# Performance work log

Measured on AMD Instinct MI355X. Metric: run time of the kernel, lower is better.

The kernel has to match this reference:

```python
import jax, jax.numpy as jnp
import numpy as np

N = 50000
E_RAND = 800000
IN, HID, OUT = 128, 64, 40
HEADS = (2, 1, 1)
NEG_SLOPE = 0.2


def setup_inputs() -> dict:
    key = jax.random.key(0)
    ks = jax.random.split(key, 16)
    # random edges with src != dst, then append self-loops (remove+add_self_loop)
    src_r = jax.random.randint(ks[0], (E_RAND,), 0, N)
    off = jax.random.randint(ks[1], (E_RAND,), 1, N)
    dst_r = (src_r + off) % N
    loops = jnp.arange(N)
    src = jnp.concatenate([src_r, loops]).astype(jnp.int64)
    dst = jnp.concatenate([dst_r, loops]).astype(jnp.int64)
    in_feat = jax.random.normal(ks[2], (N, IN), dtype=jnp.float32)

    def lin(k, fan_in, fan_out):
        return jax.random.normal(k, (fan_in, fan_out), dtype=jnp.float32) / np.sqrt(fan_in)

    H0, H1, H2 = HEADS
    # layer 0: in=IN, out=HID, heads=H0
    W0 = lin(ks[3], IN, H0 * HID)
    al0 = jax.random.normal(ks[4], (H0, HID), dtype=jnp.float32) * 0.1
    ar0 = jax.random.normal(ks[5], (H0, HID), dtype=jnp.float32) * 0.1
    b0 = jnp.zeros((H0 * HID,), dtype=jnp.float32)
    # layer 1: in=HID*H0, out=HID, heads=H1
    W1 = lin(ks[6], HID * H0, H1 * HID)
    al1 = jax.random.normal(ks[7], (H1, HID), dtype=jnp.float32) * 0.1
    ar1 = jax.random.normal(ks[8], (H1, HID), dtype=jnp.float32) * 0.1
    b1 = jnp.zeros((H1 * HID,), dtype=jnp.float32)
    # layer 2: in=HID*H1, out=OUT, heads=H2
    W2 = lin(ks[9], HID * H1, H2 * OUT)
    al2 = jax.random.normal(ks[10], (H2, OUT), dtype=jnp.float32) * 0.1
    ar2 = jax.random.normal(ks[11], (H2, OUT), dtype=jnp.float32) * 0.1
    b2 = jnp.zeros((H2 * OUT,), dtype=jnp.float32)
    return {"in_feat": in_feat, "src": src, "dst": dst,
            "W0": W0, "al0": al0, "ar0": ar0, "b0": b0,
            "W1": W1, "al1": al1, "ar1": ar1, "b1": b1,
            "W2": W2, "al2": al2, "ar2": ar2, "b2": b2}


def _gat_layer(x, src, dst, W, al, ar, b):
    # x: [N, Fin]; W: [Fin, H*D]; al/ar: [H, D]; b: [H*D]
    H, D = al.shape
    feat = (x @ W).reshape(-1, H, D)                 # [N, H, D]
    el = jnp.sum(feat * al, axis=-1)                 # [N, H]
    er = jnp.sum(feat * ar, axis=-1)                 # [N, H]
    e = jax.nn.leaky_relu(el[src] + er[dst], NEG_SLOPE)  # [E, H]
    m = jax.ops.segment_max(e, dst, num_segments=x.shape[0])
    ee = jnp.exp(e - jax.lax.stop_gradient(m)[dst])
    s = jax.ops.segment_sum(ee, dst, num_segments=x.shape[0])
    alpha = ee / s[dst]                              # softmax over in-edges per dst
    out = jax.ops.segment_sum(feat[src] * alpha[:, :, None], dst,
                              num_segments=x.shape[0])  # [N, H, D]
    return out + b.reshape(1, H, D)


def reference(in_feat, src, dst, W0, al0, ar0, b0, W1, al1, ar1, b1, W2, al2, ar2, b2):
    h = _gat_layer(in_feat, src, dst, W0, al0, ar0, b0).reshape(in_feat.shape[0], -1)  # flatten(1)
    h = _gat_layer(h, src, dst, W1, al1, ar1, b1).mean(axis=1)                          # mean over heads
    h = _gat_layer(h, src, dst, W2, al2, ar2, b2).reshape(in_feat.shape[0], -1)         # flatten(1)
    return h
```

## Files before the change

kernel.cpp:

```cpp
#include <hip/hip_runtime.h>
#include <hip/hip_fp16.h>
#include <math.h>

#define NEG_SLOPE 0.2f

typedef _Float16 h8 __attribute__((ext_vector_type(8)));
typedef float f4 __attribute__((ext_vector_type(4)));


__device__ inline float2 up2(unsigned u) {
    __half2 h;
    __builtin_memcpy(&h, &u, 4);
    return __half22float2(h);
}
__device__ inline unsigned pk2(float a, float b) {
    __half2 h = __floats2half2_rn(a, b);
    unsigned u;
    __builtin_memcpy(&u, &h, 4);
    return u;
}
__device__ inline void fma8(float* acc, const uint4& v, float p) {
    float2 f;
    f = up2(v.x); acc[0] += f.x * p; acc[1] += f.y * p;
    f = up2(v.y); acc[2] += f.x * p; acc[3] += f.y * p;
    f = up2(v.z); acc[4] += f.x * p; acc[5] += f.y * p;
    f = up2(v.w); acc[6] += f.x * p; acc[7] += f.y * p;
}
__device__ inline float dot4(const float4& a, const float4& b) {
    return a.x * b.x + a.y * b.y + a.z * b.z + a.w * b.w;
}


__global__ __launch_bounds__(256) void prep(const float* __restrict__ W0,
                                            const float* __restrict__ W1,
                                            const float* __restrict__ W2,
                                            const float* __restrict__ al2,
                                            const float* __restrict__ ar2,
                                            __half* __restrict__ P0,
                                            __half* __restrict__ P1,
                                            __half* __restrict__ P2,
                                            float* __restrict__ al2p,
                                            float* __restrict__ ar2p,
                                            int* __restrict__ deg, int N) {
    int b = blockIdx.x;
    int gtid = b * 256 + threadIdx.x;
    for (int i = gtid; i < N; i += gridDim.x * 256) deg[i] = 0;

    if (b < 14) {
        const float* W;
        __half* P;
        int K, M, Msrc, lb = b;
        if (lb < 8) {
            W = W0; P = P0; K = 128; M = 128; Msrc = 128;
        } else if (lb < 12) {
            W = W1; P = P1; K = 128; M = 64; Msrc = 64; lb -= 8;
        } else {
            W = W2; P = P2; K = 64; M = 64; Msrc = 40; lb -= 12;
        }
        int t = lb * 256 + threadIdx.x;
        int nk8 = K >> 3;
        if (t < M * nk8) {
            int m = t % M, k8 = t / M;
            int k = k8 * 8;
            int c = m >> 4, s = k >> 5, hi = (k >> 3) & 3, lane = hi * 16 + (m & 15);
            float v[8];
#pragma unroll
            for (int i = 0; i < 8; ++i)
                v[i] = (m < Msrc) ? W[(size_t)(k + i) * Msrc + m] : 0.f;
            uint4 o;
            o.x = pk2(v[0], v[1]);
            o.y = pk2(v[2], v[3]);
            o.z = pk2(v[4], v[5]);
            o.w = pk2(v[6], v[7]);
            *(uint4*)(P + (size_t)((c * (K >> 5) + s) * 64 + lane) * 8) = o;
        }
    } else if (b == 14) {
        int t = threadIdx.x;
        if (t < 64) {
            al2p[t] = (t < 40) ? al2[t] : 0.f;
            ar2p[t] = (t < 40) ? ar2[t] : 0.f;
        }
    }
}


__global__ __launch_bounds__(256) void degree_hist_rank(const int* __restrict__ dst,
                                                        int* __restrict__ deg,
                                                        int* __restrict__ rank, int E) {
    int e = blockIdx.x * blockDim.x + threadIdx.x;
    if (e >= E) return;
    int d = __builtin_nontemporal_load(&dst[e]);
    int r = atomicAdd(&deg[d], 1);
    __builtin_nontemporal_store(r, &rank[e]);
}

__global__ __launch_bounds__(256) void scan_block_sums(const int* __restrict__ in,
                                                       int* __restrict__ partial, int n) {
    int i = blockIdx.x * 256 + threadIdx.x;
    int v = (i < n) ? in[i] : 0;
#pragma unroll
    for (int off = 32; off; off >>= 1) v += __shfl_xor(v, off);
    __shared__ int wsum[4];
    if ((threadIdx.x & 63) == 0) wsum[threadIdx.x >> 6] = v;
    __syncthreads();
    if (threadIdx.x == 0) partial[blockIdx.x] = wsum[0] + wsum[1] + wsum[2] + wsum[3];
}

__global__ __launch_bounds__(256) void scan_final2(const int* __restrict__ in,
                                                   const int* __restrict__ partial,
                                                   int* __restrict__ out, int n) {
    __shared__ int buf[256];
    __shared__ int wsum[4];
    int t = threadIdx.x;
    int i = blockIdx.x * 256 + t;
    int v = (i < n) ? in[i] : 0;
    buf[t] = v;
    __syncthreads();
    for (int off = 1; off < 256; off <<= 1) {
        int x = (t >= off) ? buf[t - off] : 0;
        __syncthreads();
        buf[t] += x;
        __syncthreads();
    }
    int incl = buf[t];
    int pv = (t < blockIdx.x) ? partial[t] : 0;
#pragma unroll
    for (int off = 32; off; off >>= 1) pv += __shfl_xor(pv, off);
    if ((t & 63) == 0) wsum[t >> 6] = pv;
    __syncthreads();
    int pre = wsum[0] + wsum[1] + wsum[2] + wsum[3];
    if (i < n) out[i] = pre + incl - v;
    if (i == n - 1) out[n] = pre + incl;
}

__global__ __launch_bounds__(256) void scatter_rank(const int* __restrict__ src,
                                                    const int* __restrict__ dst,
                                                    const int* __restrict__ rank,
                                                    const int* __restrict__ row_start,
                                                    int* __restrict__ csr_src, int E) {
    int e = blockIdx.x * blockDim.x + threadIdx.x;
    if (e >= E) return;
    int d = __builtin_nontemporal_load(&dst[e]);
    int s = __builtin_nontemporal_load(&src[e]);
    int r = __builtin_nontemporal_load(&rank[e]);
    csr_src[row_start[d] + r] = s;
}


template <int K, int M, int H, bool A16>
__global__ __launch_bounds__(256) void gemm_mfma(const void* __restrict__ xin,
                                                 const __half* __restrict__ Wp,
                                                 const float* __restrict__ al,
                                                 const float* __restrict__ ar,
                                                 __half* __restrict__ outh,
                                                 float* __restrict__ el,
                                                 float* __restrict__ er, int N) {
    constexpr int KS = K / 32;
    constexpr int CF = M / 16;
    constexpr int LDT = 133;
    constexpr int CH8 = M / 8;
    constexpr int NC8 = CH8 / 4;
    __shared__ float tl[4 * 16 * LDT];
    const int tid = threadIdx.x;
    const int wid = tid >> 6, lane = tid & 63;
    const int lhi = lane >> 4, llo = lane & 15;
    const int rowbase = blockIdx.x * 64 + wid * 16;
    float* wt = tl + wid * 16 * LDT;

    f4 acc[CF];
#pragma unroll
    for (int c = 0; c < CF; ++c) acc[c] = f4{0.f, 0.f, 0.f, 0.f};

    const int arow = rowbase + llo;
    const bool aval = arow < N;
#pragma unroll
    for (int s = 0; s < KS; ++s) {
        h8 a = {};
        if (aval) {
            if constexpr (A16) {
                const __half* xp = (const __half*)xin + (size_t)arow * K + s * 32 + lhi * 8;
                a = *(const h8*)xp;
            } else {
                const float4* xp = (const float4*)((const float*)xin + (size_t)arow * K +
                                                   s * 32 + lhi * 8);
                float4 x0 = xp[0];
                float4 x1 = xp[1];
                a[0] = (_Float16)x0.x; a[1] = (_Float16)x0.y;
                a[2] = (_Float16)x0.z; a[3] = (_Float16)x0.w;
                a[4] = (_Float16)x1.x; a[5] = (_Float16)x1.y;
                a[6] = (_Float16)x1.z; a[7] = (_Float16)x1.w;
            }
        }
#pragma unroll
        for (int c = 0; c < CF; ++c) {
            h8 b = *(const h8*)(Wp + (size_t)((c * KS + s) * 64 + lane) * 8);
            acc[c] = __builtin_amdgcn_mfma_f32_16x16x32_f16(a, b, acc[c], 0, 0, 0);
        }
    }

#pragma unroll
    for (int c = 0; c < CF; ++c) {
#pragma unroll
        for (int r = 0; r < 4; ++r)
            wt[(lhi * 4 + r) * LDT + c * 16 + llo] = acc[c][r];
    }

    const int rrow = lane >> 2;
    const int q = lane & 3;
    const int grow = rowbase + rrow;
    float elp[H], erp[H];
#pragma unroll
    for (int h = 0; h < H; ++h) { elp[h] = 0.f; erp[h] = 0.f; }
    const float4* al4 = (const float4*)al;
    const float4* ar4 = (const float4*)ar;
#pragma unroll
    for (int i = 0; i < NC8; ++i) {
        int j8 = q + 4 * i;
        float4 v0 = *(float4*)&wt[rrow * LDT + 8 * j8];
        float4 v1 = *(float4*)&wt[rrow * LDT + 8 * j8 + 4];
        int h = (H == 2 && i >= NC8 / 2) ? 1 : 0;
        float4 a0 = al4[2 * j8], a1 = al4[2 * j8 + 1];
        float4 r0 = ar4[2 * j8], r1 = ar4[2 * j8 + 1];
        elp[h] += dot4(v0, a0) + dot4(v1, a1);
        erp[h] += dot4(v0, r0) + dot4(v1, r1);
        if (grow < N) {
            uint4 pkv;
            pkv.x = pk2(v0.x, v0.y);
            pkv.y = pk2(v0.z, v0.w);
            pkv.z = pk2(v1.x, v1.y);
            pkv.w = pk2(v1.z, v1.w);
            *(uint4*)(outh + (size_t)grow * M + 8 * j8) = pkv;
        }
    }
#pragma unroll
    for (int h = 0; h < H; ++h) {
#pragma unroll
        for (int off = 1; off < 4; off <<= 1) {
            elp[h] += __shfl_xor(elp[h], off);
            erp[h] += __shfl_xor(erp[h], off);
        }
    }
    if (q == 0 && grow < N) {
        if constexpr (H == 2) {
            *(float2*)&el[(size_t)grow * 2] = float2{elp[0], elp[1]};
            *(float2*)&er[(size_t)grow * 2] = float2{erp[0], erp[1]};
        } else {
            el[grow] = elp[0];
            er[grow] = erp[0];
        }
    }
}


template <int H, int D, int FSTRIDE, int T, bool OUT16>
__global__ __launch_bounds__(256) void gat_aggregate2(const __half* __restrict__ feat,
                                                      const float* __restrict__ el,
                                                      const float* __restrict__ er,
                                                      const int* __restrict__ row_start,
                                                      const int* __restrict__ csr_src,
                                                      const float* __restrict__ bias,
                                                      void* __restrict__ out, int N) {
    constexpr int NLp = FSTRIDE / 8;
    constexpr int GnH = 32 / NLp;
    constexpr int BATCH = GnH * T;
    constexpr int WL = (H * D) / 8;
    static_assert(32 % NLp == 0 && BATCH <= 32, "layout");
    int pair = (blockIdx.x * blockDim.x + threadIdx.x) >> 6;
    int lane = threadIdx.x & 63;
    if (pair * 2 >= N) return;
    const int l32 = lane & 31;
    const int hb = lane & 32;
    const int dstn = pair * 2 + (lane >> 5);
    const bool dval = dstn < N;
    int beg = dval ? row_start[dstn] : 0;
    int end = dval ? row_start[dstn + 1] : 0;
    int cnt = end - beg;

    float er_d[H];
#pragma unroll
    for (int h = 0; h < H; ++h) er_d[h] = dval ? er[(size_t)dstn * H + h] : 0.f;

    float ssum[H];
    float acc8[8];
#pragma unroll
    for (int h = 0; h < H; ++h) ssum[h] = 0.f;
#pragma unroll
    for (int i = 0; i < 8; ++i) acc8[i] = 0.f;

    const int g = l32 / NLp;
    const int ln = l32 % NLp;

    int trips = (cnt + 31) >> 5;
    {
        int to = __shfl_xor(trips, 32);
        trips = (to > trips) ? to : trips;
    }

    for (int it = 0; it < trips; ++it) {
        int base = beg + it * 32;
        int idx = base + l32;
        bool valid = idx < end;
        int s = csr_src[valid ? idx : beg];
        float p[H];
        if constexpr (H == 2) {
            float2 e2 = ((const float2*)el)[s];
            float e0 = e2.x + er_d[0];
            float e1 = e2.y + er_d[1];
            e0 = (e0 > 0.f) ? e0 : NEG_SLOPE * e0;
            e1 = (e1 > 0.f) ? e1 : NEG_SLOPE * e1;
            p[0] = valid ? __expf(e0) : 0.f;
            p[1] = valid ? __expf(e1) : 0.f;
            ssum[0] += p[0];
            ssum[1] += p[1];
        } else {
            float e = el[s] + er_d[0];
            e = (e > 0.f) ? e : NEG_SLOPE * e;
            p[0] = valid ? __expf(e) : 0.f;
            ssum[0] += p[0];
        }
        int cc = end - base;
        cc = (cc < 0) ? 0 : ((cc > 32) ? 32 : cc);
        int ccm = cc;
        {
            int o = __shfl_xor(ccm, 32);
            ccm = (o > ccm) ? o : ccm;
        }
        for (int j = 0; j < ccm; j += BATCH) {
            uint4 v[T];
#pragma unroll
            for (int t = 0; t < T; ++t) {
                if (j + GnH * t < cc) {
                    int sj = __shfl(s, hb + j + GnH * t + g);
                    v[t] = ((const uint4*)(feat + (size_t)sj * FSTRIDE))[ln];
                }
            }
#pragma unroll
            for (int t = 0; t < T; ++t) {
                if (j + GnH * t < cc) {
                    int slot = hb + j + GnH * t + g;
                    float pj = __shfl(p[0], slot);
                    if constexpr (H == 2) {
                        float pj1 = __shfl(p[1], slot);
                        pj = (ln >= 8) ? pj1 : pj;
                    }
                    fma8(acc8, v[t], pj);
                }
            }
        }
    }

#pragma unroll
    for (int h = 0; h < H; ++h)
#pragma unroll
        for (int off = 16; off; off >>= 1) ssum[h] += __shfl_xor(ssum[h], off);
#pragma unroll
    for (int i = 0; i < 8; ++i) {
#pragma unroll
        for (int off = NLp; off < 32; off <<= 1) acc8[i] += __shfl_xor(acc8[i], off);
    }
    if (l32 < WL && dval) {
        float inv;
        if constexpr (H == 2) inv = 1.f / ((l32 >= 8) ? ssum[1] : ssum[0]);
        else inv = 1.f / ssum[0];
        const float4* bp = (const float4*)bias;
        float4 bv0 = bp[2 * l32], bv1 = bp[2 * l32 + 1];
        float4 o0, o1;
        o0.x = acc8[0] * inv + bv0.x; o0.y = acc8[1] * inv + bv0.y;
        o0.z = acc8[2] * inv + bv0.z; o0.w = acc8[3] * inv + bv0.w;
        o1.x = acc8[4] * inv + bv1.x; o1.y = acc8[5] * inv + bv1.y;
        o1.z = acc8[6] * inv + bv1.z; o1.w = acc8[7] * inv + bv1.w;
        if constexpr (OUT16) {
            __half* op = (__half*)out + (size_t)dstn * (H * D);
            uint4 pkv;
            pkv.x = pk2(o0.x, o0.y);
            pkv.y = pk2(o0.z, o0.w);
            pkv.z = pk2(o1.x, o1.y);
            pkv.w = pk2(o1.z, o1.w);
            ((uint4*)op)[l32] = pkv;
        } else {
            float4* op = (float4*)((float*)out + (size_t)dstn * (H * D));
            op[2 * l32] = o0;
            op[2 * l32 + 1] = o1;
        }
    }
}


extern "C" void kernel_launch(void* const* d_in, const int* in_sizes, int n_in,
                              void* d_out, int out_size, void* d_ws, size_t ws_size,
                              hipStream_t stream) {
    const float* in_feat = (const float*)d_in[0];
    const int*   src     = (const int*)d_in[1];
    const int*   dst     = (const int*)d_in[2];
    const float* W0 = (const float*)d_in[3];
    const float* al0 = (const float*)d_in[4];
    const float* ar0 = (const float*)d_in[5];
    const float* b0 = (const float*)d_in[6];
    const float* W1 = (const float*)d_in[7];
    const float* al1 = (const float*)d_in[8];
    const float* ar1 = (const float*)d_in[9];
    const float* b1 = (const float*)d_in[10];
    const float* W2 = (const float*)d_in[11];
    const float* al2 = (const float*)d_in[12];
    const float* ar2 = (const float*)d_in[13];
    const float* b2 = (const float*)d_in[14];
    float* out = (float*)d_out;

    const int N = in_sizes[0] / 128;
    const int E = in_sizes[1];

    char* ws = (char*)d_ws;
    auto alloc = [&](size_t bytes) -> void* {
        void* p = (void*)ws;
        ws += (bytes + 255) & ~(size_t)255;
        return p;
    };
    int* deg       = (int*)alloc((size_t)N * 4);
    int* row_start = (int*)alloc((size_t)(N + 1) * 4);
    int* csr_src   = (int*)alloc((size_t)E * 4);
    int* rank      = (int*)alloc((size_t)E * 4);
    int* partial   = (int*)alloc(256 * 4);
    __half* feat   = (__half*)alloc((size_t)N * 128 * 2);
    float* el      = (float*)alloc((size_t)N * 2 * 4);
    float* er      = (float*)alloc((size_t)N * 2 * 4);
    __half* h0h    = (__half*)alloc((size_t)N * 128 * 2);
    __half* h1h    = (__half*)alloc((size_t)N * 64 * 2);
    __half* Wp0    = (__half*)alloc((size_t)128 * 128 * 2);
    __half* Wp1    = (__half*)alloc((size_t)128 * 64 * 2);
    __half* Wp2    = (__half*)alloc((size_t)64 * 64 * 2);
    float* al2p    = (float*)alloc(64 * 4);
    float* ar2p    = (float*)alloc(64 * 4);

    int egrid = (E + 255) / 256;
    int nb = (N + 255) / 256;

    prep<<<256, 256, 0, stream>>>(W0, W1, W2, al2, ar2, Wp0, Wp1, Wp2, al2p, ar2p, deg, N);
    degree_hist_rank<<<egrid, 256, 0, stream>>>(dst, deg, rank, E);
    scan_block_sums<<<nb, 256, 0, stream>>>(deg, partial, N);
    scan_final2<<<nb, 256, 0, stream>>>(deg, partial, row_start, N);
    scatter_rank<<<egrid, 256, 0, stream>>>(src, dst, rank, row_start, csr_src, E);

    int npairs = (N + 1) / 2;
    int pgrid = (npairs * 64 + 255) / 256;
    int mgrid = (N + 63) / 64;

    gemm_mfma<128, 128, 2, false><<<mgrid, 256, 0, stream>>>(in_feat, Wp0, al0, ar0, feat, el, er, N);
    gat_aggregate2<2, 64, 128, 8, true><<<pgrid, 256, 0, stream>>>(feat, el, er, row_start, csr_src, b0, h0h, N);

    gemm_mfma<128, 64, 1, true><<<mgrid, 256, 0, stream>>>(h0h, Wp1, al1, ar1, feat, el, er, N);
    gat_aggregate2<1, 64, 64, 8, true><<<pgrid, 256, 0, stream>>>(feat, el, er, row_start, csr_src, b1, h1h, N);

    gemm_mfma<64, 64, 1, true><<<mgrid, 256, 0, stream>>>(h1h, Wp2, al2p, ar2p, feat, el, er, N);
    gat_aggregate2<1, 40, 64, 8, false><<<pgrid, 256, 0, stream>>>(feat, el, er, row_start, csr_src, b2, out, N);
}
```

Measured before the change: 281.5 us.

## Fuse whole GAT pipeline into one cooperative persistent kernel with grid syncs

Replaces the chain of roughly ten separate launches (weight prep, degree histogram, scan, CSR scatter, three GEMMs and three aggregations) with a single cooperative kernel. The stages are separated by grid.sync() and use grid-stride loops, with a grid sized from occupancy and capped at 1024 blocks. The layer-0 GEMM is also placed in the same phase as the degree histogram so the two overlap. This removes per-launch overhead and the gaps between kernels, but the grid is capped and each barrier is a device-wide sync. The multi-kernel path is kept as a fallback if the cooperative launch fails.

Result: slower. 373.5 us (+32.7%).

```diff
diff --git a/kernel.cpp b/kernel.cpp
--- a/kernel.cpp
+++ b/kernel.cpp
@@ -1,6 +1,9 @@
 #include <hip/hip_runtime.h>
+#include <hip/hip_cooperative_groups.h>
 #include <hip/hip_fp16.h>
 #include <math.h>
+
+namespace cg = cooperative_groups;
 
 #define NEG_SLOPE 0.2f
 
@@ -28,6 +31,371 @@
 }
 __device__ inline float dot4(const float4& a, const float4& b) {
     return a.x * b.x + a.y * b.y + a.z * b.z + a.w * b.w;
+}
+
+
+template <int K, int M, int H, bool A16>
+__device__ void dev_gemm(float* tl_base, const void* __restrict__ xin,
+                         const __half* __restrict__ Wp,
+                         const float* __restrict__ al,
+                         const float* __restrict__ ar,
+                         __half* __restrict__ outh,
+                         float* __restrict__ el,
+                         float* __restrict__ er, int N) {
+    constexpr int KS = K / 32;
+    constexpr int CF = M / 16;
+    constexpr int LDT = 133;
+    constexpr int CH8 = M / 8;
+    constexpr int NC8 = CH8 / 4;
+    const int tid = threadIdx.x;
+    const int wid = tid >> 6, lane = tid & 63;
+    const int lhi = lane >> 4, llo = lane & 15;
+    float* wt = tl_base + wid * 16 * LDT;
+    const float4* al4 = (const float4*)al;
+    const float4* ar4 = (const float4*)ar;
+    const int ntiles = (N + 63) >> 6;
+
+    for (int tile = blockIdx.x; tile < ntiles; tile += gridDim.x) {
+        const int rowbase = tile * 64 + wid * 16;
+        f4 acc[CF];
+#pragma unroll
+        for (int c = 0; c < CF; ++c) acc[c] = f4{0.f, 0.f, 0.f, 0.f};
+
+        const int arow = rowbase + llo;
+        const bool aval = arow < N;
+#pragma unroll
+        for (int s = 0; s < KS; ++s) {
+            h8 a = {};
+            if (aval) {
+                if constexpr (A16) {
+                    const __half* xp = (const __half*)xin + (size_t)arow * K + s * 32 + lhi * 8;
+                    a = *(const h8*)xp;
+                } else {
+                    const float4* xp = (const float4*)((const float*)xin + (size_t)arow * K +
+                                                       s * 32 + lhi * 8);
+                    float4 x0 = xp[0];
+                    float4 x1 = xp[1];
+                    a[0] = (_Float16)x0.x; a[1] = (_Float16)x0.y;
+                    a[2] = (_Float16)x0.z; a[3] = (_Float16)x0.w;
+                    a[4] = (_Float16)x1.x; a[5] = (_Float16)x1.y;
+                    a[6] = (_Float16)x1.z; a[7] = (_Float16)x1.w;
+                }
+            }
+#pragma unroll
+            for (int c = 0; c < CF; ++c) {
+                h8 b = *(const h8*)(Wp + (size_t)((c * KS + s) * 64 + lane) * 8);
+                acc[c] = __builtin_amdgcn_mfma_f32_16x16x32_f16(a, b, acc[c], 0, 0, 0);
+            }
+        }
+
+#pragma unroll
+        for (int c = 0; c < CF; ++c) {
+#pragma unroll
+            for (int r = 0; r < 4; ++r)
+                wt[(lhi * 4 + r) * LDT + c * 16 + llo] = acc[c][r];
+        }
+
+        const int rrow = lane >> 2;
+        const int q = lane & 3;
+        const int grow = rowbase + rrow;
+        float elp[H], erp[H];
+#pragma unroll
+        for (int h = 0; h < H; ++h) { elp[h] = 0.f; erp[h] = 0.f; }
+#pragma unroll
+        for (int i = 0; i < NC8; ++i) {
+            int j8 = q + 4 * i;
+            float4 v0 = *(float4*)&wt[rrow * LDT + 8 * j8];
+            float4 v1 = *(float4*)&wt[rrow * LDT + 8 * j8 + 4];
+            int h = (H == 2 && i >= NC8 / 2) ? 1 : 0;
+            float4 a0 = al4[2 * j8], a1 = al4[2 * j8 + 1];
+            float4 r0 = ar4[2 * j8], r1 = ar4[2 * j8 + 1];
+            elp[h] += dot4(v0, a0) + dot4(v1, a1);
+            erp[h] += dot4(v0, r0) + dot4(v1, r1);
+            if (grow < N) {
+                uint4 pkv;
+                pkv.x = pk2(v0.x, v0.y);
+                pkv.y = pk2(v0.z, v0.w);
+                pkv.z = pk2(v1.x, v1.y);
+                pkv.w = pk2(v1.z, v1.w);
+                *(uint4*)(outh + (size_t)grow * M + 8 * j8) = pkv;
+            }
+        }
+#pragma unroll
+        for (int h = 0; h < H; ++h) {
+#pragma unroll
+            for (int off = 1; off < 4; off <<= 1) {
+                elp[h] += __shfl_xor(elp[h], off);
+                erp[h] += __shfl_xor(erp[h], off);
+            }
+        }
+        if (q == 0 && grow < N) {
+            if constexpr (H == 2) {
+                *(float2*)&el[(size_t)grow * 2] = float2{elp[0], elp[1]};
+                *(float2*)&er[(size_t)grow * 2] = float2{erp[0], erp[1]};
+            } else {
+                el[grow] = elp[0];
+                er[grow] = erp[0];
+            }
+        }
+    }
+}
+
+
+template <int H, int D, int FSTRIDE, int T, bool OUT16>
+__device__ void dev_agg(const __half* __restrict__ feat,
+                        const float* __restrict__ el,
+                        const float* __restrict__ er,
+                        const int* __restrict__ row_start,
+                        const int* __restrict__ csr_src,
+                        const float* __restrict__ bias,
+                        void* __restrict__ out, int N) {
+    constexpr int NLp = FSTRIDE / 8;
+    constexpr int GnH = 32 / NLp;
+    constexpr int BATCH = GnH * T;
+    constexpr int WL = (H * D) / 8;
+    static_assert(32 % NLp == 0 && BATCH <= 32, "layout");
+    const int lane = threadIdx.x & 63;
+    const int wid = threadIdx.x >> 6;
+    const int l32 = lane & 31;
+    const int hb = lane & 32;
+    const int g = l32 / NLp;
+    const int ln = l32 % NLp;
+    const int npairs = (N + 1) >> 1;
+
+    for (int pair = blockIdx.x * 4 + wid; pair < npairs; pair += gridDim.x * 4) {
+        const int dstn = pair * 2 + (lane >> 5);
+        const bool dval = dstn < N;
+        int beg = dval ? row_start[dstn] : 0;
+        int end = dval ? row_start[dstn + 1] : 0;
+        int cnt = end - beg;
+
+        float er_d[H];
+#pragma unroll
+        for (int h = 0; h < H; ++h) er_d[h] = dval ? er[(size_t)dstn * H + h] : 0.f;
+
+        float ssum[H];
+        float acc8[8];
+#pragma unroll
+        for (int h = 0; h < H; ++h) ssum[h] = 0.f;
+#pragma unroll
+        for (int i = 0; i < 8; ++i) acc8[i] = 0.f;
+
+        int trips = (cnt + 31) >> 5;
+        {
+            int to = __shfl_xor(trips, 32);
+            trips = (to > trips) ? to : trips;
+        }
+
+        for (int it = 0; it < trips; ++it) {
+            int base = beg + it * 32;
+            int idx = base + l32;
+            bool valid = idx < end;
+            int s = csr_src[valid ? idx : beg];
+            float p[H];
+            if constexpr (H == 2) {
+                float2 e2 = ((const float2*)el)[s];
+                float e0 = e2.x + er_d[0];
+                float e1 = e2.y + er_d[1];
+                e0 = (e0 > 0.f) ? e0 : NEG_SLOPE * e0;
+                e1 = (e1 > 0.f) ? e1 : NEG_SLOPE * e1;
+                p[0] = valid ? __expf(e0) : 0.f;
+                p[1] = valid ? __expf(e1) : 0.f;
+                ssum[0] += p[0];
+                ssum[1] += p[1];
+            } else {
+                float e = el[s] + er_d[0];
+                e = (e > 0.f) ? e : NEG_SLOPE * e;
+                p[0] = valid ? __expf(e) : 0.f;
+                ssum[0] += p[0];
+            }
+            int cc = end - base;
+            cc = (cc < 0) ? 0 : ((cc > 32) ? 32 : cc);
+            int ccm = cc;
+            {
+                int o = __shfl_xor(ccm, 32);
+                ccm = (o > ccm) ? o : ccm;
+            }
+            for (int j = 0; j < ccm; j += BATCH) {
+                uint4 v[T];
+#pragma unroll
+                for (int t = 0; t < T; ++t) {
+                    if (j + GnH * t < cc) {
+                        int sj = __shfl(s, hb + j + GnH * t + g);
+                        v[t] = ((const uint4*)(feat + (size_t)sj * FSTRIDE))[ln];
+                    }
+                }
+#pragma unroll
+                for (int t = 0; t < T; ++t) {
+                    if (j + GnH * t < cc) {
+                        int slot = hb + j + GnH * t + g;
+                        float pj = __shfl(p[0], slot);
+                        if constexpr (H == 2) {
+                            float pj1 = __shfl(p[1], slot);
+                            pj = (ln >= 8) ? pj1 : pj;
+                        }
+                        fma8(acc8, v[t], pj);
+                    }
+                }
+            }
+        }
+
+#pragma unroll
+        for (int h = 0; h < H; ++h)
+#pragma unroll
+            for (int off = 16; off; off >>= 1) ssum[h] += __shfl_xor(ssum[h], off);
+#pragma unroll
+        for (int i = 0; i < 8; ++i) {
+#pragma unroll
+            for (int off = NLp; off < 32; off <<= 1) acc8[i] += __shfl_xor(acc8[i], off);
+        }
+        if (l32 < WL && dval) {
+            float inv;
+            if constexpr (H == 2) inv = 1.f / ((l32 >= 8) ? ssum[1] : ssum[0]);
+            else inv = 1.f / ssum[0];
+            const float4* bp = (const float4*)bias;
+            float4 bv0 = bp[2 * l32], bv1 = bp[2 * l32 + 1];
+            float4 o0, o1;
+            o0.x = acc8[0] * inv + bv0.x; o0.y = acc8[1] * inv + bv0.y;
+            o0.z = acc8[2] * inv + bv0.z; o0.w = acc8[3] * inv + bv0.w;
+            o1.x = acc8[4] * inv + bv1.x; o1.y = acc8[5] * inv + bv1.y;
+            o1.z = acc8[6] * inv + bv1.z; o1.w = acc8[7] * inv + bv1.w;
+            if constexpr (OUT16) {
+                __half* op = (__half*)out + (size_t)dstn * (H * D);
+                uint4 pkv;
+                pkv.x = pk2(o0.x, o0.y);
+                pkv.y = pk2(o0.z, o0.w);
+                pkv.z = pk2(o1.x, o1.y);
+                pkv.w = pk2(o1.z, o1.w);
+                ((uint4*)op)[l32] = pkv;
+            } else {
+                float4* op = (float4*)((float*)out + (size_t)dstn * (H * D));
+                op[2 * l32] = o0;
+                op[2 * l32 + 1] = o1;
+            }
+        }
+    }
+}
+
+
+__global__ __launch_bounds__(256) void mega(
+    const float* __restrict__ in_feat, const int* __restrict__ src,
+    const int* __restrict__ dst,
+    const float* __restrict__ W0, const float* __restrict__ al0,
+    const float* __restrict__ ar0, const float* __restrict__ b0,
+    const float* __restrict__ W1, const float* __restrict__ al1,
+    const float* __restrict__ ar1, const float* __restrict__ b1,
+    const float* __restrict__ W2, const float* __restrict__ al2,
+    const float* __restrict__ ar2, const float* __restrict__ b2,
+    float* __restrict__ out,
+    int* __restrict__ deg, int* __restrict__ row_start,
+    int* __restrict__ csr_src, int* __restrict__ rank, int* __restrict__ partial,
+    __half* __restrict__ feat, float* __restrict__ el, float* __restrict__ er,
+    __half* __restrict__ h0h, __half* __restrict__ h1h,
+    __half* __restrict__ Wp0, __half* __restrict__ Wp1, __half* __restrict__ Wp2,
+    float* __restrict__ al2p, float* __restrict__ ar2p, int N, int E) {
+    cg::grid_group grid = cg::this_grid();
+    __shared__ float sm_f[4 * 16 * 133];
+    int* sm_i = (int*)sm_f;
+    const int t = threadIdx.x;
+    const int gt = blockIdx.x * 256 + t;
+    const int gsz = gridDim.x * 256;
+
+    for (int i = gt; i < N; i += gsz) deg[i] = 0;
+    if (blockIdx.x < 14) {
+        const float* W;
+        __half* P;
+        int K, M, Msrc, lb = blockIdx.x;
+        if (lb < 8) {
+            W = W0; P = Wp0; K = 128; M = 128; Msrc = 128;
+        } else if (lb < 12) {
+            W = W1; P = Wp1; K = 128; M = 64; Msrc = 64; lb -= 8;
+        } else {
+            W = W2; P = Wp2; K = 64; M = 64; Msrc = 40; lb -= 12;
+        }
+        int tt = lb * 256 + t;
+        int nk8 = K >> 3;
+        if (tt < M * nk8) {
+            int m = tt % M, k8 = tt / M;
+            int k = k8 * 8;
+            int c = m >> 4, s = k >> 5, hi = (k >> 3) & 3, lane = hi * 16 + (m & 15);
+            float v[8];
+#pragma unroll
+            for (int i = 0; i < 8; ++i)
+                v[i] = (m < Msrc) ? W[(size_t)(k + i) * Msrc + m] : 0.f;
+            uint4 o;
+            o.x = pk2(v[0], v[1]);
+            o.y = pk2(v[2], v[3]);
+            o.z = pk2(v[4], v[5]);
+            o.w = pk2(v[6], v[7]);
+            *(uint4*)(P + (size_t)((c * (K >> 5) + s) * 64 + lane) * 8) = o;
+        }
+    } else if (blockIdx.x == 14 && t < 64) {
+        al2p[t] = (t < 40) ? al2[t] : 0.f;
+        ar2p[t] = (t < 40) ? ar2[t] : 0.f;
+    }
+    grid.sync();
+
+    dev_gemm<128, 128, 2, false>(sm_f, in_feat, Wp0, al0, ar0, feat, el, er, N);
+    for (int e = gt; e < E; e += gsz) {
+        int d = dst[e];
+        rank[e] = atomicAdd(&deg[d], 1);
+    }
+    grid.sync();
+
+    for (int b = blockIdx.x; b * 256 < N; b += gridDim.x) {
+        int i = b * 256 + t;
+        int v = (i < N) ? deg[i] : 0;
+#pragma unroll
+        for (int off = 32; off; off >>= 1) v += __shfl_xor(v, off);
+        if ((t & 63) == 0) sm_i[256 + (t >> 6)] = v;
+        __syncthreads();
+        if (t == 0) partial[b] = sm_i[256] + sm_i[257] + sm_i[258] + sm_i[259];
+        __syncthreads();
+    }
+    grid.sync();
+
+    for (int b = blockIdx.x; b * 256 < N; b += gridDim.x) {
+        int i = b * 256 + t;
+        int v = (i < N) ? deg[i] : 0;
+        sm_i[t] = v;
+        __syncthreads();
+        for (int off = 1; off < 256; off <<= 1) {
+            int x = (t >= off) ? sm_i[t - off] : 0;
+            __syncthreads();
+            sm_i[t] += x;
+            __syncthreads();
+        }
+        int incl = sm_i[t];
+        int pv = (t < b) ? partial[t] : 0;
+#pragma unroll
+        for (int off = 32; off; off >>= 1) pv += __shfl_xor(pv, off);
+        if ((t & 63) == 0) sm_i[256 + (t >> 6)] = pv;
+        __syncthreads();
+        int pre = sm_i[256] + sm_i[257] + sm_i[258] + sm_i[259];
+        if (i < N) row_start[i] = pre + incl - v;
+        if (i == N - 1) row_start[N] = pre + incl;
+        __syncthreads();
+    }
+    grid.sync();
+
+    for (int e = gt; e < E; e += gsz) {
+        csr_src[row_start[dst[e]] + rank[e]] = src[e];
+    }
+    grid.sync();
+
+    dev_agg<2, 64, 128, 8, true>(feat, el, er, row_start, csr_src, b0, h0h, N);
+    grid.sync();
+
+    dev_gemm<128, 64, 1, true>(sm_f, h0h, Wp1, al1, ar1, feat, el, er, N);
+    grid.sync();
+
+    dev_agg<1, 64, 64, 8, true>(feat, el, er, row_start, csr_src, b1, h1h, N);
+    grid.sync();
+
+    dev_gemm<64, 64, 1, true>(sm_f, h1h, Wp2, al2p, ar2p, feat, el, er, N);
+    grid.sync();
+
+    dev_agg<1, 40, 64, 8, false>(feat, el, er, row_start, csr_src, b2, out, N);
 }
 
 
@@ -82,7 +450,6 @@
         }
     }
 }
-
 
 __global__ __launch_bounds__(256) void degree_hist_rank(const int* __restrict__ dst,
                                                         int* __restrict__ deg,
@@ -146,7 +513,6 @@
     csr_src[row_start[d] + r] = s;
 }
 
-
 template <int K, int M, int H, bool A16>
 __global__ __launch_bounds__(256) void gemm_mfma(const void* __restrict__ xin,
                                                  const __half* __restrict__ Wp,
@@ -155,102 +521,9 @@
                                                  __half* __restrict__ outh,
                                                  float* __restrict__ el,
                                                  float* __restrict__ er, int N) {
-    constexpr int KS = K / 32;
-    constexpr int CF = M / 16;
-    constexpr int LDT = 133;
-    constexpr int CH8 = M / 8;
-    constexpr int NC8 = CH8 / 4;
-    __shared__ float tl[4 * 16 * LDT];
-    const int tid = threadIdx.x;
-    const int wid = tid >> 6, lane = tid & 63;
-    const int lhi = lane >> 4, llo = lane & 15;
-    const int rowbase = blockIdx.x * 64 + wid * 16;
-    float* wt = tl + wid * 16 * LDT;
-
-    f4 acc[CF];
-#pragma unroll
-    for (int c = 0; c < CF; ++c) acc[c] = f4{0.f, 0.f, 0.f, 0.f};
-
-    const int arow = rowbase + llo;
-    const bool aval = arow < N;
-#pragma unroll
-    for (int s = 0; s < KS; ++s) {
-        h8 a = {};
-        if (aval) {
-            if constexpr (A16) {
-                const __half* xp = (const __half*)xin + (size_t)arow * K + s * 32 + lhi * 8;
-                a = *(const h8*)xp;
-            } else {
-                const float4* xp = (const float4*)((const float*)xin + (size_t)arow * K +
-                                                   s * 32 + lhi * 8);
-                float4 x0 = xp[0];
-                float4 x1 = xp[1];
-                a[0] = (_Float16)x0.x; a[1] = (_Float16)x0.y;
-                a[2] = (_Float16)x0.z; a[3] = (_Float16)x0.w;
-                a[4] = (_Float16)x1.x; a[5] = (_Float16)x1.y;
-                a[6] = (_Float16)x1.z; a[7] = (_Float16)x1.w;
-            }
-        }
-#pragma unroll
-        for (int c = 0; c < CF; ++c) {
-            h8 b = *(const h8*)(Wp + (size_t)((c * KS + s) * 64 + lane) * 8);
-            acc[c] = __builtin_amdgcn_mfma_f32_16x16x32_f16(a, b, acc[c], 0, 0, 0);
-        }
-    }
-
-#pragma unroll
-    for (int c = 0; c < CF; ++c) {
-#pragma unroll
-        for (int r = 0; r < 4; ++r)
-            wt[(lhi * 4 + r) * LDT + c * 16 + llo] = acc[c][r];
-    }
-
-    const int rrow = lane >> 2;
-    const int q = lane & 3;
-    const int grow = rowbase + rrow;
-    float elp[H], erp[H];
-#pragma unroll
-    for (int h = 0; h < H; ++h) { elp[h] = 0.f; erp[h] = 0.f; }
-    const float4* al4 = (const float4*)al;
-    const float4* ar4 = (const float4*)ar;
-#pragma unroll
-    for (int i = 0; i < NC8; ++i) {
-        int j8 = q + 4 * i;
-        float4 v0 = *(float4*)&wt[rrow * LDT + 8 * j8];
-        float4 v1 = *(float4*)&wt[rrow * LDT + 8 * j8 + 4];
-        int h = (H == 2 && i >= NC8 / 2) ? 1 : 0;
-        float4 a0 = al4[2 * j8], a1 = al4[2 * j8 + 1];
-        float4 r0 = ar4[2 * j8], r1 = ar4[2 * j8 + 1];
-        elp[h] += dot4(v0, a0) + dot4(v1, a1);
-        erp[h] += dot4(v0, r0) + dot4(v1, r1);
-        if (grow < N) {
-            uint4 pkv;
-            pkv.x = pk2(v0.x, v0.y);
-            pkv.y = pk2(v0.z, v0.w);
-            pkv.z = pk2(v1.x, v1.y);
-            pkv.w = pk2(v1.z, v1.w);
-            *(uint4*)(outh + (size_t)grow * M + 8 * j8) = pkv;
-        }
-    }
-#pragma unroll
-    for (int h = 0; h < H; ++h) {
-#pragma unroll
-        for (int off = 1; off < 4; off <<= 1) {
-            elp[h] += __shfl_xor(elp[h], off);
-            erp[h] += __shfl_xor(erp[h], off);
-        }
-    }
-    if (q == 0 && grow < N) {
-        if constexpr (H == 2) {
-            *(float2*)&el[(size_t)grow * 2] = float2{elp[0], elp[1]};
-            *(float2*)&er[(size_t)grow * 2] = float2{erp[0], erp[1]};
-        } else {
-            el[grow] = elp[0];
-            er[grow] = erp[0];
-        }
-    }
-}
-
+    __shared__ float tl[4 * 16 * 133];
+    dev_gemm<K, M, H, A16>(tl, xin, Wp, al, ar, outh, el, er, N);
+}
 
 template <int H, int D, int FSTRIDE, int T, bool OUT16>
 __global__ __launch_bounds__(256) void gat_aggregate2(const __half* __restrict__ feat,
@@ -260,129 +533,7 @@
                                                       const int* __restrict__ csr_src,
                                                       const float* __restrict__ bias,
                                                       void* __restrict__ out, int N) {
-    constexpr int NLp = FSTRIDE / 8;
-    constexpr int GnH = 32 / NLp;
-    constexpr int BATCH = GnH * T;
-    constexpr int WL = (H * D) / 8;
-    static_assert(32 % NLp == 0 && BATCH <= 32, "layout");
-    int pair = (blockIdx.x * blockDim.x + threadIdx.x) >> 6;
-    int lane = threadIdx.x & 63;
-    if (pair * 2 >= N) return;
-    const int l32 = lane & 31;
-    const int hb = lane & 32;
-    const int dstn = pair * 2 + (lane >> 5);
-    const bool dval = dstn < N;
-    int beg = dval ? row_start[dstn] : 0;
-    int end = dval ? row_start[dstn + 1] : 0;
-    int cnt = end - beg;
-
-    float er_d[H];
-#pragma unroll
-    for (int h = 0; h < H; ++h) er_d[h] = dval ? er[(size_t)dstn * H + h] : 0.f;
-
-    float ssum[H];
-    float acc8[8];
-#pragma unroll
-    for (int h = 0; h < H; ++h) ssum[h] = 0.f;
-#pragma unroll
-    for (int i = 0; i < 8; ++i) acc8[i] = 0.f;
-
-    const int g = l32 / NLp;
-    const int ln = l32 % NLp;
-
-    int trips = (cnt + 31) >> 5;
-    {
-        int to = __shfl_xor(trips, 32);
-        trips = (to > trips) ? to : trips;
-    }
-
-    for (int it = 0; it < trips; ++it) {
-        int base = beg + it * 32;
-        int idx = base + l32;
-        bool valid = idx < end;
-        int s = csr_src[valid ? idx : beg];
-        float p[H];
-        if constexpr (H == 2) {
-            float2 e2 = ((const float2*)el)[s];
-            float e0 = e2.x + er_d[0];
-            float e1 = e2.y + er_d[1];
-            e0 = (e0 > 0.f) ? e0 : NEG_SLOPE * e0;
-            e1 = (e1 > 0.f) ? e1 : NEG_SLOPE * e1;
-            p[0] = valid ? __expf(e0) : 0.f;
-            p[1] = valid ? __expf(e1) : 0.f;
-            ssum[0] += p[0];
-            ssum[1] += p[1];
-        } else {
-            float e = el[s] + er_d[0];
-            e = (e > 0.f) ? e : NEG_SLOPE * e;
-            p[0] = valid ? __expf(e) : 0.f;
-            ssum[0] += p[0];
-        }
-        int cc = end - base;
-        cc = (cc < 0) ? 0 : ((cc > 32) ? 32 : cc);
-        int ccm = cc;
-        {
-            int o = __shfl_xor(ccm, 32);
-            ccm = (o > ccm) ? o : ccm;
-        }
-        for (int j = 0; j < ccm; j += BATCH) {
-            uint4 v[T];
-#pragma unroll
-            for (int t = 0; t < T; ++t) {
-                if (j + GnH * t < cc) {
-                    int sj = __shfl(s, hb + j + GnH * t + g);
-                    v[t] = ((const uint4*)(feat + (size_t)sj * FSTRIDE))[ln];
-                }
-            }
-#pragma unroll
-            for (int t = 0; t < T; ++t) {
-                if (j + GnH * t < cc) {
-                    int slot = hb + j + GnH * t + g;
-                    float pj = __shfl(p[0], slot);
-                    if constexpr (H == 2) {
-                        float pj1 = __shfl(p[1], slot);
-                        pj = (ln >= 8) ? pj1 : pj;
-                    }
-                    fma8(acc8, v[t], pj);
-                }
-            }
-        }
-    }
-
-#pragma unroll
-    for (int h = 0; h < H; ++h)
-#pragma unroll
-        for (int off = 16; off; off >>= 1) ssum[h] += __shfl_xor(ssum[h], off);
-#pragma unroll
-    for (int i = 0; i < 8; ++i) {
-#pragma unroll
-        for (int off = NLp; off < 32; off <<= 1) acc8[i] += __shfl_xor(acc8[i], off);
-    }
-    if (l32 < WL && dval) {
-        float inv;
-        if constexpr (H == 2) inv = 1.f / ((l32 >= 8) ? ssum[1] : ssum[0]);
-        else inv = 1.f / ssum[0];
-        const float4* bp = (const float4*)bias;
-        float4 bv0 = bp[2 * l32], bv1 = bp[2 * l32 + 1];
-        float4 o0, o1;
-        o0.x = acc8[0] * inv + bv0.x; o0.y = acc8[1] * inv + bv0.y;
-        o0.z = acc8[2] * inv + bv0.z; o0.w = acc8[3] * inv + bv0.w;
-        o1.x = acc8[4] * inv + bv1.x; o1.y = acc8[5] * inv + bv1.y;
-        o1.z = acc8[6] * inv + bv1.z; o1.w = acc8[7] * inv + bv1.w;
-        if constexpr (OUT16) {
-            __half* op = (__half*)out + (size_t)dstn * (H * D);
-            uint4 pkv;
-            pkv.x = pk2(o0.x, o0.y);
-            pkv.y = pk2(o0.z, o0.w);
-            pkv.z = pk2(o1.x, o1.y);
-            pkv.w = pk2(o1.z, o1.w);
-            ((uint4*)op)[l32] = pkv;
-        } else {
-            float4* op = (float4*)((float*)out + (size_t)dstn * (H * D));
-            op[2 * l32] = o0;
-            op[2 * l32 + 1] = o1;
-        }
-    }
+    dev_agg<H, D, FSTRIDE, T, OUT16>(feat, el, er, row_start, csr_src, bias, out, N);
 }
 
 
@@ -431,6 +582,43 @@
     float* al2p    = (float*)alloc(64 * 4);
     float* ar2p    = (float*)alloc(64 * 4);
 
+    static int coop_grid = -2;
+    if (coop_grid == -2) {
+        int dev_sup = 0;
+        if (hipDeviceGetAttribute(&dev_sup, hipDeviceAttributeCooperativeLaunch, 0) !=
+                hipSuccess ||
+            !dev_sup) {
+            coop_grid = 0;
+        } else {
+            int per_cu = 0;
+            hipError_t e =
+                hipOccupancyMaxActiveBlocksPerMultiprocessor(&per_cu, mega, 256, 0);
+            if (e != hipSuccess || per_cu <= 0) {
+                coop_grid = 0;
+            } else {
+                coop_grid = per_cu * 256;
+                if (coop_grid > 1024) coop_grid = 1024;
+            }
+        }
+    }
+    if (coop_grid > 0) {
+        void* args[] = {
+            (void*)&in_feat, (void*)&src, (void*)&dst,
+            (void*)&W0, (void*)&al0, (void*)&ar0, (void*)&b0,
+            (void*)&W1, (void*)&al1, (void*)&ar1, (void*)&b1,
+            (void*)&W2, (void*)&al2, (void*)&ar2, (void*)&b2,
+            (void*)&out,
+            (void*)&deg, (void*)&row_start, (void*)&csr_src, (void*)&rank,
+            (void*)&partial,
+            (void*)&feat, (void*)&el, (void*)&er, (void*)&h0h, (void*)&h1h,
+            (void*)&Wp0, (void*)&Wp1, (void*)&Wp2, (void*)&al2p, (void*)&ar2p,
+            (void*)&N, (void*)&E};
+        hipError_t e = hipLaunchCooperativeKernel((const void*)mega, dim3(coop_grid),
+                                                  dim3(256), args, 0, stream);
+        if (e == hipSuccess) return;
+        coop_grid = 0;
+    }
+
     int egrid = (E + 255) / 256;
     int nb = (N + 255) / 256;
 
```

## Fuse aggregation with next-layer GEMM and merge CSR scatter with first GEMM

Applied to the files above, without the earlier changes.

Each aggregation kernel now writes its fp16 output tile into swizzled LDS, and the same block runs the next layer's MFMA GEMM on it. This removes the h0/h1 global round-trips and two kernel launches. The CSR build switches from a rank array to atomic cursors, and that scatter is fused into the layer-0 GEMM kernel. The cost is a nondeterministic neighbour order within each CSR row, lower parallelism in the agg_gemm kernels (one block per 64 nodes, 8 serial iterations per wave), and possible load imbalance.

After: 332.1 us. +18.0%, slower.

```diff
diff --git a/kernel.cpp b/kernel.cpp
--- a/kernel.cpp
+++ b/kernel.cpp
@@ -84,14 +84,11 @@
 }
 
 
-__global__ __launch_bounds__(256) void degree_hist_rank(const int* __restrict__ dst,
-                                                        int* __restrict__ deg,
-                                                        int* __restrict__ rank, int E) {
+__global__ __launch_bounds__(256) void hist(const int* __restrict__ dst,
+                                            int* __restrict__ deg, int E) {
     int e = blockIdx.x * blockDim.x + threadIdx.x;
     if (e >= E) return;
-    int d = __builtin_nontemporal_load(&dst[e]);
-    int r = atomicAdd(&deg[d], 1);
-    __builtin_nontemporal_store(r, &rank[e]);
+    atomicAdd(&deg[__builtin_nontemporal_load(&dst[e])], 1);
 }
 
 __global__ __launch_bounds__(256) void scan_block_sums(const int* __restrict__ in,
@@ -106,9 +103,10 @@
     if (threadIdx.x == 0) partial[blockIdx.x] = wsum[0] + wsum[1] + wsum[2] + wsum[3];
 }
 
-__global__ __launch_bounds__(256) void scan_final2(const int* __restrict__ in,
+__global__ __launch_bounds__(256) void scan_final3(const int* __restrict__ in,
                                                    const int* __restrict__ partial,
-                                                   int* __restrict__ out, int n) {
+                                                   int* __restrict__ out,
+                                                   int* __restrict__ cursor, int n) {
     __shared__ int buf[256];
     __shared__ int wsum[4];
     int t = threadIdx.x;
@@ -129,43 +127,30 @@
     if ((t & 63) == 0) wsum[t >> 6] = pv;
     __syncthreads();
     int pre = wsum[0] + wsum[1] + wsum[2] + wsum[3];
-    if (i < n) out[i] = pre + incl - v;
+    if (i < n) {
+        int rs = pre + incl - v;
+        out[i] = rs;
+        cursor[i] = rs;
+    }
     if (i == n - 1) out[n] = pre + incl;
 }
 
-__global__ __launch_bounds__(256) void scatter_rank(const int* __restrict__ src,
-                                                    const int* __restrict__ dst,
-                                                    const int* __restrict__ rank,
-                                                    const int* __restrict__ row_start,
-                                                    int* __restrict__ csr_src, int E) {
-    int e = blockIdx.x * blockDim.x + threadIdx.x;
-    if (e >= E) return;
-    int d = __builtin_nontemporal_load(&dst[e]);
-    int s = __builtin_nontemporal_load(&src[e]);
-    int r = __builtin_nontemporal_load(&rank[e]);
-    csr_src[row_start[d] + r] = s;
-}
-
-
-template <int K, int M, int H, bool A16>
-__global__ __launch_bounds__(256) void gemm_mfma(const void* __restrict__ xin,
-                                                 const __half* __restrict__ Wp,
-                                                 const float* __restrict__ al,
-                                                 const float* __restrict__ ar,
-                                                 __half* __restrict__ outh,
-                                                 float* __restrict__ el,
-                                                 float* __restrict__ er, int N) {
+
+template <int K, int M, int H, int AMODE, int LSTR>
+__device__ __forceinline__ void gemm_tile(float* wt, const void* __restrict__ xin,
+                                          const __half* aw,
+                                          const __half* __restrict__ Wp,
+                                          const float* __restrict__ al,
+                                          const float* __restrict__ ar,
+                                          __half* __restrict__ outh,
+                                          float* __restrict__ el,
+                                          float* __restrict__ er, int rowbase, int N) {
     constexpr int KS = K / 32;
     constexpr int CF = M / 16;
-    constexpr int LDT = 133;
-    constexpr int CH8 = M / 8;
-    constexpr int NC8 = CH8 / 4;
-    __shared__ float tl[4 * 16 * LDT];
-    const int tid = threadIdx.x;
-    const int wid = tid >> 6, lane = tid & 63;
+    constexpr int LDT = (M == 128) ? 133 : 69;
+    constexpr int NC8 = (M / 8) / 4;
+    const int lane = threadIdx.x & 63;
     const int lhi = lane >> 4, llo = lane & 15;
-    const int rowbase = blockIdx.x * 64 + wid * 16;
-    float* wt = tl + wid * 16 * LDT;
 
     f4 acc[CF];
 #pragma unroll
@@ -176,11 +161,14 @@
 #pragma unroll
     for (int s = 0; s < KS; ++s) {
         h8 a = {};
-        if (aval) {
-            if constexpr (A16) {
-                const __half* xp = (const __half*)xin + (size_t)arow * K + s * 32 + lhi * 8;
-                a = *(const h8*)xp;
-            } else {
+        if constexpr (AMODE == 2) {
+            int c8 = s * 4 + lhi;
+            a = *(const h8*)(aw + llo * LSTR + ((c8 ^ (llo & 7)) << 3));
+        } else if constexpr (AMODE == 1) {
+            if (aval)
+                a = *(const h8*)((const __half*)xin + (size_t)arow * K + s * 32 + lhi * 8);
+        } else {
+            if (aval) {
                 const float4* xp = (const float4*)((const float*)xin + (size_t)arow * K +
                                                    s * 32 + lhi * 8);
                 float4 x0 = xp[0];
@@ -197,6 +185,7 @@
             acc[c] = __builtin_amdgcn_mfma_f32_16x16x32_f16(a, b, acc[c], 0, 0, 0);
         }
     }
+    asm volatile("" ::: "memory");
 
 #pragma unroll
     for (int c = 0; c < CF; ++c) {
@@ -204,6 +193,7 @@
         for (int r = 0; r < 4; ++r)
             wt[(lhi * 4 + r) * LDT + c * 16 + llo] = acc[c][r];
     }
+    asm volatile("" ::: "memory");
 
     const int rrow = lane >> 2;
     const int q = lane & 3;
@@ -252,26 +242,25 @@
 }
 
 
-template <int H, int D, int FSTRIDE, int T, bool OUT16>
-__global__ __launch_bounds__(256) void gat_aggregate2(const __half* __restrict__ feat,
-                                                      const float* __restrict__ el,
-                                                      const float* __restrict__ er,
-                                                      const int* __restrict__ row_start,
-                                                      const int* __restrict__ csr_src,
-                                                      const float* __restrict__ bias,
-                                                      void* __restrict__ out, int N) {
+template <int H, int D, int FSTRIDE, int T>
+__device__ __forceinline__ void agg_one(const __half* __restrict__ feat,
+                                        const float* __restrict__ el,
+                                        const float* __restrict__ er,
+                                        const int* __restrict__ row_start,
+                                        const int* __restrict__ csr_src,
+                                        const float* __restrict__ bias,
+                                        int dstn, bool dval, int lane,
+                                        float4& o0, float4& o1) {
     constexpr int NLp = FSTRIDE / 8;
     constexpr int GnH = 32 / NLp;
     constexpr int BATCH = GnH * T;
     constexpr int WL = (H * D) / 8;
     static_assert(32 % NLp == 0 && BATCH <= 32, "layout");
-    int pair = (blockIdx.x * blockDim.x + threadIdx.x) >> 6;
-    int lane = threadIdx.x & 63;
-    if (pair * 2 >= N) return;
     const int l32 = lane & 31;
     const int hb = lane & 32;
-    const int dstn = pair * 2 + (lane >> 5);
-    const bool dval = dstn < N;
+    const int g = l32 / NLp;
+    const int ln = l32 % NLp;
+
     int beg = dval ? row_start[dstn] : 0;
     int end = dval ? row_start[dstn + 1] : 0;
     int cnt = end - beg;
@@ -286,9 +275,6 @@
     for (int h = 0; h < H; ++h) ssum[h] = 0.f;
 #pragma unroll
     for (int i = 0; i < 8; ++i) acc8[i] = 0.f;
-
-    const int g = l32 / NLp;
-    const int ln = l32 % NLp;
 
     int trips = (cnt + 31) >> 5;
     {
@@ -358,30 +344,117 @@
 #pragma unroll
         for (int off = NLp; off < 32; off <<= 1) acc8[i] += __shfl_xor(acc8[i], off);
     }
-    if (l32 < WL && dval) {
-        float inv;
-        if constexpr (H == 2) inv = 1.f / ((l32 >= 8) ? ssum[1] : ssum[0]);
-        else inv = 1.f / ssum[0];
+    o0 = float4{0.f, 0.f, 0.f, 0.f};
+    o1 = float4{0.f, 0.f, 0.f, 0.f};
+    if (l32 < WL) {
+        float sden;
+        if constexpr (H == 2) sden = (l32 >= 8) ? ssum[1] : ssum[0];
+        else sden = ssum[0];
+        float inv = (dval && sden > 0.f) ? 1.f / sden : 0.f;
+        float bsc = dval ? 1.f : 0.f;
         const float4* bp = (const float4*)bias;
         float4 bv0 = bp[2 * l32], bv1 = bp[2 * l32 + 1];
+        o0.x = (acc8[0] * inv + bv0.x) * bsc; o0.y = (acc8[1] * inv + bv0.y) * bsc;
+        o0.z = (acc8[2] * inv + bv0.z) * bsc; o0.w = (acc8[3] * inv + bv0.w) * bsc;
+        o1.x = (acc8[4] * inv + bv1.x) * bsc; o1.y = (acc8[5] * inv + bv1.y) * bsc;
+        o1.z = (acc8[6] * inv + bv1.z) * bsc; o1.w = (acc8[7] * inv + bv1.w) * bsc;
+    }
+}
+
+
+__global__ __launch_bounds__(256) void scatter_gemm0(
+    const int* __restrict__ src, const int* __restrict__ dst,
+    int* __restrict__ cursor, int* __restrict__ csr_src,
+    const float* __restrict__ in_feat, const __half* __restrict__ Wp0,
+    const float* __restrict__ al0, const float* __restrict__ ar0,
+    __half* __restrict__ feat0, float* __restrict__ el0, float* __restrict__ er0,
+    int N, int E) {
+    constexpr int LDT = 133;
+    __shared__ float tl[4 * 16 * LDT];
+    const int wid = threadIdx.x >> 6;
+    const int ntiles = (N + 63) >> 6;
+    if (blockIdx.x < ntiles) {
+        gemm_tile<128, 128, 2, 0, 0>(tl + wid * 16 * LDT, in_feat, nullptr, Wp0, al0,
+                                     ar0, feat0, el0, er0, blockIdx.x * 64 + wid * 16,
+                                     N);
+    }
+    int e = blockIdx.x * 256 + threadIdx.x;
+    if (e < E) {
+        int d = __builtin_nontemporal_load(&dst[e]);
+        int s = __builtin_nontemporal_load(&src[e]);
+        int pos = atomicAdd(&cursor[d], 1);
+        csr_src[pos] = s;
+    }
+}
+
+
+template <int HA, int DA, int FSA, int T, int KG, int LSTR>
+__global__ __launch_bounds__(256, 4) void agg_gemm(
+    const __half* __restrict__ featA, const float* __restrict__ elA,
+    const float* __restrict__ erA, const int* __restrict__ row_start,
+    const int* __restrict__ csr_src, const float* __restrict__ biasA,
+    const __half* __restrict__ Wp, const float* __restrict__ alG,
+    const float* __restrict__ arG, __half* __restrict__ featO,
+    float* __restrict__ elO, float* __restrict__ erO, int N) {
+    constexpr int LDT = 69;
+    constexpr int REGB = 16 * LDT * 4;
+    static_assert(16 * LSTR * 2 <= REGB, "h-tile must fit region");
+    static_assert(HA * DA == KG, "agg out feeds gemm K");
+    constexpr int WL = (HA * DA) / 8;
+    __shared__ alignas(16) char smem[4][REGB];
+    const int lane = threadIdx.x & 63;
+    const int wid = threadIdx.x >> 6;
+    const int l32 = lane & 31;
+    __half* lds_h = (__half*)&smem[wid][0];
+    float* wt = (float*)&smem[wid][0];
+    const int dbase = blockIdx.x * 64 + wid * 16;
+
+#pragma unroll 1
+    for (int it = 0; it < 8; ++it) {
+        int dl = it * 2 + (lane >> 5);
+        int dstn = dbase + dl;
+        bool dval = dstn < N;
         float4 o0, o1;
-        o0.x = acc8[0] * inv + bv0.x; o0.y = acc8[1] * inv + bv0.y;
-        o0.z = acc8[2] * inv + bv0.z; o0.w = acc8[3] * inv + bv0.w;
-        o1.x = acc8[4] * inv + bv1.x; o1.y = acc8[5] * inv + bv1.y;
-        o1.z = acc8[6] * inv + bv1.z; o1.w = acc8[7] * inv + bv1.w;
-        if constexpr (OUT16) {
-            __half* op = (__half*)out + (size_t)dstn * (H * D);
+        agg_one<HA, DA, FSA, T>(featA, elA, erA, row_start, csr_src, biasA, dstn,
+                                dval, lane, o0, o1);
+        if (l32 < WL) {
             uint4 pkv;
             pkv.x = pk2(o0.x, o0.y);
             pkv.y = pk2(o0.z, o0.w);
             pkv.z = pk2(o1.x, o1.y);
             pkv.w = pk2(o1.z, o1.w);
-            ((uint4*)op)[l32] = pkv;
-        } else {
-            float4* op = (float4*)((float*)out + (size_t)dstn * (H * D));
-            op[2 * l32] = o0;
-            op[2 * l32 + 1] = o1;
-        }
+            ((uint4*)(lds_h + dl * LSTR))[l32 ^ (dl & 7)] = pkv;
+        }
+    }
+    asm volatile("" ::: "memory");
+
+    gemm_tile<KG, 64, 1, 2, LSTR>(wt, nullptr, lds_h, Wp, alG, arG, featO, elO, erO,
+                                  dbase, N);
+}
+
+
+template <int H, int D, int FSTRIDE, int T>
+__global__ __launch_bounds__(256) void gat_agg_out(const __half* __restrict__ feat,
+                                                   const float* __restrict__ el,
+                                                   const float* __restrict__ er,
+                                                   const int* __restrict__ row_start,
+                                                   const int* __restrict__ csr_src,
+                                                   const float* __restrict__ bias,
+                                                   float* __restrict__ out, int N) {
+    int pair = (blockIdx.x * blockDim.x + threadIdx.x) >> 6;
+    int lane = threadIdx.x & 63;
+    if (pair * 2 >= N) return;
+    int dstn = pair * 2 + (lane >> 5);
+    bool dval = dstn < N;
+    float4 o0, o1;
+    agg_one<H, D, FSTRIDE, T>(feat, el, er, row_start, csr_src, bias, dstn, dval,
+                              lane, o0, o1);
+    constexpr int WL = (H * D) / 8;
+    int l32 = lane & 31;
+    if (l32 < WL && dval) {
+        float4* op = (float4*)(out + (size_t)dstn * (H * D));
+        op[2 * l32] = o0;
+        op[2 * l32 + 1] = o1;
     }
 }
 
@@ -417,14 +490,18 @@
     };
     int* deg       = (int*)alloc((size_t)N * 4);
     int* row_start = (int*)alloc((size_t)(N + 1) * 4);
+    int* cursor    = (int*)alloc((size_t)N * 4);
     int* csr_src   = (int*)alloc((size_t)E * 4);
-    int* rank      = (int*)alloc((size_t)E * 4);
     int* partial   = (int*)alloc(256 * 4);
-    __half* feat   = (__half*)alloc((size_t)N * 128 * 2);
-    float* el      = (float*)alloc((size_t)N * 2 * 4);
-    float* er      = (float*)alloc((size_t)N * 2 * 4);
-    __half* h0h    = (__half*)alloc((size_t)N * 128 * 2);
-    __half* h1h    = (__half*)alloc((size_t)N * 64 * 2);
+    __half* feat0  = (__half*)alloc((size_t)N * 128 * 2);
+    float* el0     = (float*)alloc((size_t)N * 2 * 4);
+    float* er0     = (float*)alloc((size_t)N * 2 * 4);
+    __half* feat1  = (__half*)alloc((size_t)N * 64 * 2);
+    float* el1     = (float*)alloc((size_t)N * 4);
+    float* er1     = (float*)alloc((size_t)N * 4);
+    __half* feat2  = (__half*)alloc((size_t)N * 64 * 2);
+    float* el2     = (float*)alloc((size_t)N * 4);
+    float* er2     = (float*)alloc((size_t)N * 4);
     __half* Wp0    = (__half*)alloc((size_t)128 * 128 * 2);
     __half* Wp1    = (__half*)alloc((size_t)128 * 64 * 2);
     __half* Wp2    = (__half*)alloc((size_t)64 * 64 * 2);
@@ -433,23 +510,20 @@
 
     int egrid = (E + 255) / 256;
     int nb = (N + 255) / 256;
-
-    prep<<<256, 256, 0, stream>>>(W0, W1, W2, al2, ar2, Wp0, Wp1, Wp2, al2p, ar2p, deg, N);
-    degree_hist_rank<<<egrid, 256, 0, stream>>>(dst, deg, rank, E);
+    int ntiles = (N + 63) / 64;
+    int pgrid = (((N + 1) / 2) * 64 + 255) / 256;
+
+    prep<<<256, 256, 0, stream>>>(W0, W1, W2, al2, ar2, Wp0, Wp1, Wp2, al2p, ar2p,
+                                  deg, N);
+    hist<<<egrid, 256, 0, stream>>>(dst, deg, E);
     scan_block_sums<<<nb, 256, 0, stream>>>(deg, partial, N);
-    scan_final2<<<nb, 256, 0, stream>>>(deg, partial, row_start, N);
-    scatter_rank<<<egrid, 256, 0, stream>>>(src, dst, rank, row_start, csr_src, E);
-
-    int npairs = (N + 1) / 2;
-    int pgrid = (npairs * 64 + 255) / 256;
-    int mgrid = (N + 63) / 64;
-
-    gemm_mfma<128, 128, 2, false><<<mgrid, 256, 0, stream>>>(in_feat, Wp0, al0, ar0, feat, el, er, N);
-    gat_aggregate2<2, 64, 128, 8, true><<<pgrid, 256, 0, stream>>>(feat, el, er, row_start, csr_src, b0, h0h, N);
-
-    gemm_mfma<128, 64, 1, true><<<mgrid, 256, 0, stream>>>(h0h, Wp1, al1, ar1, feat, el, er, N);
-    gat_aggregate2<1, 64, 64, 8, true><<<pgrid, 256, 0, stream>>>(feat, el, er, row_start, csr_src, b1, h1h, N);
-
-    gemm_mfma<64, 64, 1, true><<<mgrid, 256, 0, stream>>>(h1h, Wp2, al2p, ar2p, feat, el, er, N);
-    gat_aggregate2<1, 40, 64, 8, false><<<pgrid, 256, 0, stream>>>(feat, el, er, row_start, csr_src, b2, out, N);
-}
+    scan_final3<<<nb, 256, 0, stream>>>(deg, partial, row_start, cursor, N);
+    scatter_gemm0<<<egrid, 256, 0, stream>>>(src, dst, cursor, csr_src, in_feat, Wp0,
+                                             al0, ar0, feat0, el0, er0, N, E);
+    agg_gemm<2, 64, 128, 8, 128, 136><<<ntiles, 256, 0, stream>>>(
+        feat0, el0, er0, row_start, csr_src, b0, Wp1, al1, ar1, feat1, el1, er1, N);
+    agg_gemm<1, 64, 64, 8, 64, 72><<<ntiles, 256, 0, stream>>>(
+        feat1, el1, er1, row_start, csr_src, b1, Wp2, al2p, ar2p, feat2, el2, er2, N);
+    gat_agg_out<1, 40, 64, 8><<<pgrid, 256, 0, stream>>>(feat2, el2, er2, row_start,
+                                                         csr_src, b2, out, N);
+}
```
